# Performance work log

Hardware: AMD Instinct MI355X
Metric: run time of the kernel (lower is better)

The kernel has to match this reference:

```python
import jax, jax.numpy as jnp
import numpy as np

DIM = 64; Hh = 128; Ww = 128; Bz = 4
N = 8      # d_state
R = 4      # dt_rank = ceil(dim/16)
K = 4      # depthwise conv kernel
NB = 4     # number of CrossMambaBlocks (spa, spe, spa_cross, spe_cross)


def setup_inputs() -> dict:
    key = jax.random.key(0)
    ks = jax.random.split(key, 16)
    f32 = jnp.float32
    D = DIM
    rn = lambda k, shp, s: jax.random.normal(k, shp, f32) * s
    inp = {
        "img1": rn(ks[0], (Bz, D, Hh, Ww), 1.0),
        "img2": rn(ks[1], (Bz, D, Hh, Ww), 1.0),
        "img1_sum": rn(ks[2], (Bz, D, Hh, Ww), 1.0),
        "img2_sum": rn(ks[3], (Bz, D, Hh, Ww), 1.0),
        # LayerNorm params for norm0/norm1 of each block
        "ln_g0": jnp.ones((NB, D), f32), "ln_b0": jnp.zeros((NB, D), f32),
        "ln_g1": jnp.ones((NB, D), f32), "ln_b1": jnp.zeros((NB, D), f32),
        # Mamba projections (in_proj -> x,z from input0; in_proj_e -> extra embedding path)
        "W_in": rn(ks[4], (NB, D, 2 * D), D ** -0.5),
        "W_ine": rn(ks[5], (NB, D, D), D ** -0.5),
        # per-direction depthwise causal conv
        "convW": rn(ks[6], (NB, 2, D, K), K ** -0.5),
        "convB": jnp.zeros((NB, 2, D), f32),
        # x_proj (dt, B, C) computed from the cross-modal embedding (v7 cross variant)
        "W_x": rn(ks[7], (NB, 2, D, R + 2 * N), D ** -0.5),
        "W_dt": rn(ks[8], (NB, 2, R, D), R ** -0.5),
        "b_dt": jnp.full((NB, 2, D), -4.6, f32),  # softplus ~ 0.01
        "A_log": jnp.log(jnp.broadcast_to(jnp.arange(1, N + 1, dtype=f32), (NB, 2, D, N))),
        "Dp": jnp.ones((NB, 2, D), f32),
        "W_out": rn(ks[9], (NB, D, D), D ** -0.5),
        "b_out": jnp.zeros((NB, D), f32),
        # FusionMamba.out_proj
        "W_fo": rn(ks[10], (D, D), D ** -0.5),
        "b_fo": jnp.zeros((D,), f32),
    }
    return inp


def _ln(x, g, b):
    m = x.mean(-1, keepdims=True)
    v = ((x - m) ** 2).mean(-1, keepdims=True)
    return (x - m) * jax.lax.rsqrt(v + 1e-5) * g + b


def _causal_conv(x, w, b):
    # x: [B, L, D], w: [D, K] depthwise causal conv
    xt = x.transpose(0, 2, 1)  # [B, D, L]
    out = jax.lax.conv_general_dilated(xt, w[:, None, :], (1,), [(K - 1, 0)],
                                       feature_group_count=w.shape[0])
    return out.transpose(0, 2, 1) + b


def _selective_scan(x, dt, Bm, Cm, A):
    # x, dt: [B, L, D]; Bm, Cm: [B, L, N]; A: [D, N]
    def step(h, t):
        x_t, dt_t, B_t, C_t = t  # [B,D],[B,D],[B,N],[B,N]
        dA = jnp.exp(dt_t[:, :, None] * A)                       # [B,D,N]
        h = h * dA + (dt_t * x_t)[:, :, None] * B_t[:, None, :]  # [B,D,N]
        y = jnp.einsum('bdn,bn->bd', h, C_t)
        return h, y
    h0 = jnp.zeros((x.shape[0], x.shape[2], A.shape[1]), x.dtype)
    xs = (x.transpose(1, 0, 2), dt.transpose(1, 0, 2),
          Bm.transpose(1, 0, 2), Cm.transpose(1, 0, 2))
    _, ys = jax.lax.scan(step, h0, xs)
    return ys.transpose(1, 0, 2)  # [B, L, D]


def _cross_mamba_block(x0, x1, i, p):
    # x0, x1: [B, L, D]; bidirectional cross Mamba (bimamba v7, sum of directions)
    skip = x0
    a = _ln(x0, p['ln_g0'][i], p['ln_b0'][i])
    e = _ln(x1, p['ln_g1'][i], p['ln_b1'][i])
    xz = a @ p['W_in'][i]
    x, z = jnp.split(xz, 2, axis=-1)
    ee = e @ p['W_ine'][i]  # cross-modal embedding drives dt/B/C
    y = 0.0
    for d in range(2):
        xd = x if d == 0 else x[:, ::-1]
        ed = ee if d == 0 else ee[:, ::-1]
        zd = z if d == 0 else z[:, ::-1]
        xc = jax.nn.silu(_causal_conv(xd, p['convW'][i, d], p['convB'][i, d]))
        dbl = ed @ p['W_x'][i, d]
        dtr, Bm, Cm = dbl[..., :R], dbl[..., R:R + N], dbl[..., R + N:]
        dt = jax.nn.softplus(dtr @ p['W_dt'][i, d] + p['b_dt'][i, d])
        A = -jnp.exp(p['A_log'][i, d])
        yd = _selective_scan(xc, dt, Bm, Cm, A) + xc * p['Dp'][i, d]
        yd = yd * jax.nn.silu(zd)
        if d == 1:
            yd = yd[:, ::-1]
        y = y + yd
    return y @ p['W_out'][i] + p['b_out'][i] + skip


def reference(img1, img2, img1_sum, img2_sum, ln_g0, ln_b0, ln_g1, ln_b1,
              W_in, W_ine, convW, convB, W_x, W_dt, b_dt, A_log, Dp,
              W_out, b_out, W_fo, b_fo):
    p = dict(ln_g0=ln_g0, ln_b0=ln_b0, ln_g1=ln_g1, ln_b1=ln_b1, W_in=W_in,
             W_ine=W_ine, convW=convW, convB=convB, W_x=W_x, W_dt=W_dt,
             b_dt=b_dt, A_log=A_log, Dp=Dp, W_out=W_out, b_out=b_out)
    b, c, h, w = img1.shape
    flat = lambda t: t.reshape(b, c, h * w).transpose(0, 2, 1)   # b c h w -> b (hw) c
    unflat = lambda t: t.transpose(0, 2, 1).reshape(b, c, h, w)
    x1, x2, s1, s2 = flat(img1), flat(img2), flat(img1_sum), flat(img2_sum)
    x1 = _cross_mamba_block(x1, s1, 0, p)  # spa layer
    x2 = _cross_mamba_block(x2, s2, 1, p)  # spe layer
    spa = _cross_mamba_block(x1, x2, 2, p)
    spe = _cross_mamba_block(x2, x1, 3, p)
    fusion = (spa + spe) @ W_fo + b_fo
    out = unflat(fusion)
    return (unflat(x1) + out, unflat(x2) + out, img1_sum, img2_sum)
```

## Files before the change

### kernel.cpp

```cpp
#include <hip/hip_runtime.h>
#include <hip/hip_bf16.h>

#define BZ 4
#define DD 64
#define LL 16384
#define NN 8
#define BLD ((size_t)BZ*DD*LL)
#define BML ((size_t)BZ*20*LL)

__device__ __forceinline__ float silu_(float x){ return __fdividef(x, 1.f + __expf(-x)); }
__device__ __forceinline__ float softplus_(float x){ return (x > 20.f) ? x : __logf(1.f + __expf(x)); }


__global__ __launch_bounds__(256)
void k_tr(const float* __restrict__ t0, const float* __restrict__ t1,
          const float* __restrict__ t2, const float* __restrict__ t3,
          float* __restrict__ d0, float* __restrict__ d1,
          float* __restrict__ d2, float* __restrict__ d3)
{
  __shared__ float tile[64][65];
  const int tid = blockIdx.x;
  const int tsr = tid >> 10;
  const int rem = tid & 1023;
  const int b  = rem >> 8;
  const int l0 = (rem & 255) << 6;
  const float* s = (tsr==0)?t0:(tsr==1)?t1:(tsr==2)?t2:t3;
  float*       d = (tsr==0)?d0:(tsr==1)?d1:(tsr==2)?d2:d3;
  const int w = threadIdx.x >> 6, lane = threadIdx.x & 63;
  #pragma unroll
  for (int i=0;i<16;++i){
    const int ch = w*16+i;
    tile[ch][lane] = s[((size_t)(b*DD+ch))*LL + l0 + lane];
  }
  __syncthreads();
  #pragma unroll
  for (int i=0;i<16;++i){
    const int lw = w*16+i;
    d[((size_t)b*LL + l0+lw)*DD + lane] = tile[lane][lw];
  }
}

__global__ __launch_bounds__(256)
void k_in2(const float* __restrict__ s0a, const float* __restrict__ s1a,
           const float* __restrict__ s0b, const float* __restrict__ s1b,
           const float* __restrict__ lng0, const float* __restrict__ lnb0,
           const float* __restrict__ lng1, const float* __restrict__ lnb1,
           const float* __restrict__ W_in, const float* __restrict__ W_ine,
           const float* __restrict__ W_x, int i0,
           float* __restrict__ XBa, float* __restrict__ ZBa,
           float* __restrict__ XBb, float* __restrict__ ZBb,
           float* __restrict__ M00, float* __restrict__ M01,
           float* __restrict__ M10, float* __restrict__ M11)
{
  const int sel  = blockIdx.x >> 8;
  const int pi   = sel / 3;
  const int role = sel - 3*pi;
  const int pos = (blockIdx.x & 255)*256 + threadIdx.x;
  const int b = pos >> 14;
  const int l = pos & (LL-1);
  const int i = i0 + pi;
  const size_t row = ((size_t)b*LL + l)*DD;

  if (role < 2){
    const float* src0 = pi ? s0b : s0a;
    float a[DD];
    {
      const float4* s4 = (const float4*)(src0 + row);
      #pragma unroll
      for (int q=0;q<16;++q){ float4 v=s4[q]; a[4*q]=v.x; a[4*q+1]=v.y; a[4*q+2]=v.z; a[4*q+3]=v.w; }
    }
    float m=0.f;
    #pragma unroll
    for (int k=0;k<DD;++k) m += a[k];
    m *= (1.f/DD);
    float v=0.f;
    #pragma unroll
    for (int k=0;k<DD;++k){ float d=a[k]-m; v += d*d; }
    v *= (1.f/DD);
    const float rs = rsqrtf(v + 1e-5f);
    #pragma unroll
    for (int k=0;k<DD;++k) a[k] = (a[k]-m)*rs*lng0[i*DD+k] + lnb0[i*DD+k];

    const float* Wi = W_in + (size_t)i*DD*2*DD;
    float* drow = ((role==0) ? (pi ? XBb : XBa) : (pi ? ZBb : ZBa)) + row;
    const int gbase = role*4;
    for (int g=0; g<4; ++g){
      float acc[16];
      #pragma unroll
      for (int j=0;j<16;++j) acc[j]=0.f;
      #pragma unroll
      for (int k=0;k<DD;++k){
        const float av = a[k];
        const float* wr = Wi + k*128 + (gbase+g)*16;
        #pragma unroll
        for (int j=0;j<16;++j) acc[j] = fmaf(av, wr[j], acc[j]);
      }
      #pragma unroll
      for (int q=0;q<4;++q)
        ((float4*)(drow + g*16))[q] = make_float4(acc[4*q],acc[4*q+1],acc[4*q+2],acc[4*q+3]);
    }
  } else {
    const float* src1 = pi ? s1b : s1a;
    float e[DD];
    {
      const float4* s4 = (const float4*)(src1 + row);
      #pragma unroll
      for (int q=0;q<16;++q){ float4 v=s4[q]; e[4*q]=v.x; e[4*q+1]=v.y; e[4*q+2]=v.z; e[4*q+3]=v.w; }
    }
    float m=0.f;
    #pragma unroll
    for (int k=0;k<DD;++k) m += e[k];
    m *= (1.f/DD);
    float v=0.f;
    #pragma unroll
    for (int k=0;k<DD;++k){ float d=e[k]-m; v += d*d; }
    v *= (1.f/DD);
    const float rs = rsqrtf(v + 1e-5f);
    #pragma unroll
    for (int k=0;k<DD;++k) e[k] = (e[k]-m)*rs*lng1[i*DD+k] + lnb1[i*DD+k];

    const float* We  = W_ine + (size_t)i*DD*DD;
    const float* Wx0 = W_x + ((size_t)(i*2+0)*DD)*20;
    const float* Wx1 = W_x + ((size_t)(i*2+1)*DD)*20;
    float acc0[20], acc1[20];
    #pragma unroll
    for (int j=0;j<20;++j){ acc0[j]=0.f; acc1[j]=0.f; }
    for (int gg=0; gg<4; ++gg){
      float eeg[16];
      #pragma unroll
      for (int j=0;j<16;++j) eeg[j]=0.f;
      #pragma unroll
      for (int k=0;k<DD;++k){
        const float ev = e[k];
        const float* wr = We + k*DD + gg*16;
        #pragma unroll
        for (int j=0;j<16;++j) eeg[j] = fmaf(ev, wr[j], eeg[j]);
      }
      const float* w0 = Wx0 + (size_t)(gg*16)*20;
      const float* w1 = Wx1 + (size_t)(gg*16)*20;
      #pragma unroll
      for (int jj=0;jj<16;++jj){
        const float s = eeg[jj];
        #pragma unroll
        for (int j=0;j<20;++j){
          acc0[j] = fmaf(s, w0[jj*20+j], acc0[j]);
          acc1[j] = fmaf(s, w1[jj*20+j], acc1[j]);
        }
      }
    }
    float* mrow0 = (pi ? M10 : M00) + ((size_t)b*LL + l)*20;
    float* mrow1 = (pi ? M11 : M01) + ((size_t)b*LL + l)*20;
    #pragma unroll
    for (int q=0;q<5;++q){
      ((float4*)mrow0)[q] = make_float4(acc0[4*q],acc0[4*q+1],acc0[4*q+2],acc0[4*q+3]);
      ((float4*)mrow1)[q] = make_float4(acc1[4*q],acc1[4*q+1],acc1[4*q+2],acc1[4*q+3]);
    }
  }
}

template<int NC2, bool PASSC>
__global__ __launch_bounds__(64)
void k_scan4(const float* __restrict__ XBa, const float* __restrict__ XBb,
             const float* __restrict__ ZBa, const float* __restrict__ ZBb,
             float* __restrict__ Y0, float* __restrict__ Y1,
             float* __restrict__ Y2, float* __restrict__ Y3,
             const float* __restrict__ M00, const float* __restrict__ M01,
             const float* __restrict__ M10, const float* __restrict__ M11,
             const float* __restrict__ convW, const float* __restrict__ convB,
             const float* __restrict__ Wdt, const float* __restrict__ bdt,
             const float* __restrict__ Alog, const float* __restrict__ Dpw, int i0,
             float* __restrict__ PP, float* __restrict__ FF,
             const float* __restrict__ HH)
{
  const int TC2 = LL / NC2;
  const size_t SC2 = (size_t)BZ*NC2*DD*NN;
  const int inst = blockIdx.x / (BZ*NC2);
  const int rb = blockIdx.x - inst*(BZ*NC2);
  const int c = rb & (NC2-1);
  const int b = rb / NC2;
  const int ch = threadIdx.x;
  const int pi = inst >> 1, d = inst & 1;
  const int id = (i0+pi)*2 + d;

  const float* xb = pi ? XBb : XBa;
  const float* zb = pi ? ZBb : ZBa;
  const float* meta = (inst==0)?M00:(inst==1)?M01:(inst==2)?M10:M11;
  float* yb = (inst==0)?Y0:(inst==1)?Y1:(inst==2)?Y2:Y3;

  float cw[4];
  #pragma unroll
  for (int k=0;k<4;++k) cw[k] = convW[((size_t)id*DD+ch)*4 + k];
  const float cb = convB[id*DD + ch];
  float wd[4];
  #pragma unroll
  for (int r=0;r<4;++r) wd[r] = Wdt[((size_t)id*4 + r)*DD + ch];
  const float bd = bdt[id*DD + ch];
  float An[NN];
  #pragma unroll
  for (int n=0;n<NN;++n) An[n] = -__expf(Alog[((size_t)id*DD+ch)*NN + n]);
  const float dp = PASSC ? Dpw[id*DD + ch] : 0.f;

  bool fastA = true;
  #pragma unroll
  for (int n=0;n<NN;++n) fastA = fastA && (fabsf(An[n] + (float)(n+1)) < 1e-3f);

  const size_t sbase = (size_t)inst*SC2 + ((size_t)(b*NC2+c)*DD + ch)*NN;
  float h[NN], P[NN];
  float Sdt = 0.f;
  if (PASSC){
    #pragma unroll
    for (int n=0;n<NN;++n) h[n] = HH[sbase+n];
  } else {
    #pragma unroll
    for (int n=0;n<NN;++n){ h[n]=0.f; P[n]=1.f; }
  }

  const int stp = d ? -1 : 1;
  const int t0  = d ? (LL-1 - c*TC2) : (c*TC2);

  float p1=0.f, p2=0.f, p3=0.f;
  {
    int tp = t0 - stp;
    if ((unsigned)tp < LL) p1 = xb[((size_t)b*LL+tp)*DD+ch];
    tp -= stp;
    if ((unsigned)tp < LL) p2 = xb[((size_t)b*LL+tp)*DD+ch];
    tp -= stp;
    if ((unsigned)tp < LL) p3 = xb[((size_t)b*LL+tp)*DD+ch];
  }

  int t = t0;
  for (int s=0; s<TC2; ++s, t+=stp){
    const size_t row = (size_t)b*LL + t;
    const float xv = xb[row*DD+ch];
    const float xc = silu_(cb + cw[0]*p3 + cw[1]*p2 + cw[2]*p1 + cw[3]*xv);
    p3=p2; p2=p1; p1=xv;

    const float* mt = meta + row*20;
    const float dpre = bd + mt[0]*wd[0] + mt[1]*wd[1] + mt[2]*wd[2] + mt[3]*wd[3];
    const float dt = softplus_(dpre);
    const float u = dt*xc;

    float dA[NN];
    if (fastA){
      const float E = __expf(-dt);
      const float E2 = E*E, E4 = E2*E2;
      dA[0]=E;    dA[1]=E2;    dA[2]=E2*E;  dA[3]=E4;
      dA[4]=E4*E; dA[5]=E4*E2; dA[6]=E4*E2*E; dA[7]=E4*E4;
      Sdt += dt;
    } else {
      #pragma unroll
      for (int n=0;n<NN;++n) dA[n] = __expf(dt*An[n]);
    }

    if (!PASSC){
      #pragma unroll
      for (int n=0;n<NN;++n) h[n] = fmaf(h[n], dA[n], u*mt[4+n]);
      if (!fastA){
        #pragma unroll
        for (int n=0;n<NN;++n) P[n] *= dA[n];
      }
    } else {
      float y = 0.f;
      #pragma unroll
      for (int n=0;n<NN;++n){
        h[n] = fmaf(h[n], dA[n], u*mt[4+n]);
        y = fmaf(h[n], mt[12+n], y);
      }
      const float zv = zb[row*DD+ch];
      yb[row*DD + ch] = (y + xc*dp)*silu_(zv);
    }
  }

  if (!PASSC){
    if (fastA){
      const float E = __expf(-Sdt);
      const float E2 = E*E, E4 = E2*E2;
      P[0]=E;    P[1]=E2;    P[2]=E2*E;  P[3]=E4;
      P[4]=E4*E; P[5]=E4*E2; P[6]=E4*E2*E; P[7]=E4*E4;
    }
    #pragma unroll
    for (int n=0;n<NN;++n){ PP[sbase+n] = P[n]; FF[sbase+n] = h[n]; }
  }
}

template<int NC2>
__global__ __launch_bounds__(256)
void k_mid4(const float* __restrict__ PP, const float* __restrict__ FF,
            float* __restrict__ HH)
{
  const size_t SC2 = (size_t)BZ*NC2*DD*NN;
  const int inst = blockIdx.x >> 3;
  const int idx = (blockIdx.x & 7)*256 + threadIdx.x;
  const int b  = idx >> 9;
  const int cn = idx & 511;
  const size_t base = (size_t)inst*SC2;
  float h = 0.f;
  #pragma unroll 4
  for (int c=0; c<NC2; ++c){
    const size_t a2 = base + (((size_t)(b*NC2+c))<<9) + cn;
    HH[a2] = h;
    h = h*PP[a2] + FF[a2];
  }
}

__global__ __launch_bounds__(256)
void k_out2(const float* __restrict__ Y0, const float* __restrict__ Y1,
            const float* __restrict__ Y2, const float* __restrict__ Y3,
            const float* __restrict__ skipA, const float* __restrict__ skipB,
            const float* __restrict__ Wout, const float* __restrict__ bout,
            float* __restrict__ dstA, float* __restrict__ dstB)
{
  const int sel = blockIdx.x >> 8;
  const int pi = sel >> 2;
  const int g  = sel & 3;
  const int pos = (blockIdx.x & 255)*256 + threadIdx.x;
  const int b = pos >> 14;
  const int l = pos & (LL-1);
  const size_t row = ((size_t)b*LL + l)*DD;

  const float* Ya = pi ? Y2 : Y0;
  const float* Yb = pi ? Y3 : Y1;
  const float* skip = pi ? skipB : skipA;
  float* dst = pi ? dstB : dstA;
  const float* Wo = Wout + (size_t)pi*DD*DD;
  const float* bo = bout + pi*DD;

  float y[DD];
  {
    const float4* pa = (const float4*)(Ya + row);
    const float4* pb = (const float4*)(Yb + row);
    #pragma unroll
    for (int q=0;q<16;++q){
      float4 v0=pa[q], v1=pb[q];
      y[4*q]=v0.x+v1.x; y[4*q+1]=v0.y+v1.y; y[4*q+2]=v0.z+v1.z; y[4*q+3]=v0.w+v1.w;
    }
  }
  float acc[16];
  #pragma unroll
  for (int j=0;j<16;++j) acc[j]=0.f;
  #pragma unroll
  for (int k=0;k<DD;++k){
    const float av = y[k];
    const float* wr = Wo + k*DD + g*16;
    #pragma unroll
    for (int j=0;j<16;++j) acc[j] = fmaf(av, wr[j], acc[j]);
  }
  const float4* sk4 = (const float4*)(skip + row + g*16);
  float4* d4 = (float4*)(dst + row + g*16);
  #pragma unroll
  for (int q=0;q<4;++q){
    float4 sv = sk4[q];
    float4 v;
    v.x = acc[4*q+0] + bo[g*16+4*q+0] + sv.x;
    v.y = acc[4*q+1] + bo[g*16+4*q+1] + sv.y;
    v.z = acc[4*q+2] + bo[g*16+4*q+2] + sv.z;
    v.w = acc[4*q+3] + bo[g*16+4*q+3] + sv.w;
    d4[q] = v;
  }
}

__global__ __launch_bounds__(256)
void k_o34(const float* __restrict__ Y0, const float* __restrict__ Y1,
           const float* __restrict__ Y2, const float* __restrict__ Y3,
           const float* __restrict__ X1, const float* __restrict__ X2,
           const float* __restrict__ Wout, const float* __restrict__ bout,
           float* __restrict__ FSa, float* __restrict__ FSb)
{
  const int sel = blockIdx.x >> 8;
  const int wh = sel >> 2;
  const int g  = sel & 3;
  const int pos = (blockIdx.x & 255)*256 + threadIdx.x;
  const int b = pos >> 14;
  const int l = pos & (LL-1);
  const size_t row = ((size_t)b*LL + l)*DD;

  const float* Ya = wh ? Y2 : Y0;
  const float* Yb = wh ? Y3 : Y1;
  const float* skip = wh ? X2 : X1;
  float* FS = wh ? FSb : FSa;
  const float* Wo = Wout + (size_t)(2+wh)*DD*DD;
  const float* bo = bout + (2+wh)*DD;

  float y[DD];
  {
    const float4* pa = (const float4*)(Ya + row);
    const float4* pb = (const float4*)(Yb + row);
    #pragma unroll
    for (int q=0;q<16;++q){
      float4 v0=pa[q], v1=pb[q];
      y[4*q]=v0.x+v1.x; y[4*q+1]=v0.y+v1.y; y[4*q+2]=v0.z+v1.z; y[4*q+3]=v0.w+v1.w;
    }
  }
  float acc[16];
  #pragma unroll
  for (int j=0;j<16;++j) acc[j]=0.f;
  #pragma unroll
  for (int k=0;k<DD;++k){
    const float av = y[k];
    const float* wr = Wo + k*DD + g*16;
    #pragma unroll
    for (int j=0;j<16;++j) acc[j] = fmaf(av, wr[j], acc[j]);
  }
  const float4* sk4 = (const float4*)(skip + row + g*16);
  float4* f4 = (float4*)(FS + row + g*16);
  #pragma unroll
  for (int q=0;q<4;++q){
    float4 sv = sk4[q];
    float4 v;
    v.x = acc[4*q+0] + bo[g*16+4*q+0] + sv.x;
    v.y = acc[4*q+1] + bo[g*16+4*q+1] + sv.y;
    v.z = acc[4*q+2] + bo[g*16+4*q+2] + sv.z;
    v.w = acc[4*q+3] + bo[g*16+4*q+3] + sv.w;
    f4[q] = v;
  }
}

__global__ __launch_bounds__(256)
void k_fuse2(const float* __restrict__ FSa, const float* __restrict__ FSb,
             const float* __restrict__ X1, const float* __restrict__ X2,
             const float* __restrict__ Wfo, const float* __restrict__ bfo,
             float* __restrict__ ob)
{
  const int g = blockIdx.x >> 8;
  const int pos = (blockIdx.x & 255)*256 + threadIdx.x;
  const int b = pos >> 14;
  const int l = pos & (LL-1);
  const size_t row = ((size_t)b*LL + l)*DD;

  float fs[DD];
  {
    const float4* pa = (const float4*)(FSa + row);
    const float4* pb = (const float4*)(FSb + row);
    #pragma unroll
    for (int q=0;q<16;++q){
      float4 v0=pa[q], v1=pb[q];
      fs[4*q]=v0.x+v1.x; fs[4*q+1]=v0.y+v1.y; fs[4*q+2]=v0.z+v1.z; fs[4*q+3]=v0.w+v1.w;
    }
  }
  float acc[16];
  #pragma unroll
  for (int j=0;j<16;++j) acc[j]=0.f;
  #pragma unroll
  for (int k=0;k<DD;++k){
    const float av = fs[k];
    const float* wr = Wfo + k*DD + g*16;
    #pragma unroll
    for (int j=0;j<16;++j) acc[j] = fmaf(av, wr[j], acc[j]);
  }
  float x1v[16], x2v[16];
  {
    const float4* p1 = (const float4*)(X1 + row + g*16);
    const float4* p2 = (const float4*)(X2 + row + g*16);
    #pragma unroll
    for (int q=0;q<4;++q){
      float4 v1=p1[q], v2=p2[q];
      x1v[4*q]=v1.x; x1v[4*q+1]=v1.y; x1v[4*q+2]=v1.z; x1v[4*q+3]=v1.w;
      x2v[4*q]=v2.x; x2v[4*q+1]=v2.y; x2v[4*q+2]=v2.z; x2v[4*q+3]=v2.w;
    }
  }
  #pragma unroll
  for (int j=0;j<16;++j){
    const int col = g*16 + j;
    const size_t o = ((size_t)(b*DD+col))*LL + l;
    const float fu = acc[j] + bfo[col];
    ob[o]       = x1v[j] + fu;
    ob[BLD + o] = x2v[j] + fu;
  }
}

__global__ __launch_bounds__(256)
void k_copyboth(const float* __restrict__ s1, const float* __restrict__ s2,
                float* __restrict__ o)
{
  const size_t gid = (size_t)blockIdx.x*256 + threadIdx.x;
  const size_t half = BLD/4;
  if (gid < half) ((float4*)(o        ))[gid]        = ((const float4*)s1)[gid];
  else            ((float4*)(o + BLD ))[gid - half]  = ((const float4*)s2)[gid - half];
}

__global__ __launch_bounds__(256)
void k_copy4(const float* __restrict__ s, float* __restrict__ o)
{
  const size_t i = (size_t)blockIdx.x*256 + threadIdx.x;
  ((float4*)o)[i] = ((const float4*)s)[i];
}

__global__ __launch_bounds__(256)
void f_in(const float* __restrict__ src0, const float* __restrict__ src1,
          const float* __restrict__ lng0, const float* __restrict__ lnb0,
          const float* __restrict__ lng1, const float* __restrict__ lnb1,
          const float* __restrict__ W_in, const float* __restrict__ W_ine,
          const float* __restrict__ W_x, int i,
          float* __restrict__ XB, float* __restrict__ ZB,
          float* __restrict__ M0, float* __restrict__ M1)
{
  const int gid = blockIdx.x*256 + threadIdx.x;
  const int b = gid >> 14;
  const int l = gid & (LL-1);

  float a[DD];
  for (int ch=0; ch<DD; ++ch) a[ch] = src0[((size_t)(b*DD+ch))*LL + l];
  {
    float m=0.f; for (int k=0;k<DD;++k) m += a[k];  m *= (1.f/DD);
    float v=0.f; for (int k=0;k<DD;++k){ float d=a[k]-m; v += d*d; }  v *= (1.f/DD);
    float rs = rsqrtf(v + 1e-5f);
    for (int k=0;k<DD;++k) a[k] = (a[k]-m)*rs*lng0[i*DD+k] + lnb0[i*DD+k];
  }
  const float* Wi = W_in + (size_t)i*DD*2*DD;
  float* xrow = XB + ((size_t)b*LL + l)*DD;
  float* zrow = ZB + ((size_t)b*LL + l)*DD;
  for (int g=0; g<8; ++g){
    float acc[16];
    #pragma unroll
    for (int j=0;j<16;++j) acc[j]=0.f;
    for (int k=0;k<DD;++k){
      const float av = a[k];
      const float* wr = Wi + k*128 + g*16;
      #pragma unroll
      for (int j=0;j<16;++j) acc[j] = fmaf(av, wr[j], acc[j]);
    }
    float* drow = (g<4) ? (xrow + g*16) : (zrow + (g-4)*16);
    #pragma unroll
    for (int q=0;q<4;++q)
      ((float4*)drow)[q] = make_float4(acc[4*q],acc[4*q+1],acc[4*q+2],acc[4*q+3]);
  }
  float e[DD], ee[DD];
  for (int ch=0; ch<DD; ++ch) e[ch] = src1[((size_t)(b*DD+ch))*LL + l];
  {
    float m=0.f; for (int k=0;k<DD;++k) m += e[k];  m *= (1.f/DD);
    float v=0.f; for (int k=0;k<DD;++k){ float d=e[k]-m; v += d*d; }  v *= (1.f/DD);
    float rs = rsqrtf(v + 1e-5f);
    for (int k=0;k<DD;++k) e[k] = (e[k]-m)*rs*lng1[i*DD+k] + lnb1[i*DD+k];
  }
  const float* We = W_ine + (size_t)i*DD*DD;
  for (int m2=0; m2<DD; ++m2){
    float s = 0.f;
    for (int k=0;k<DD;++k) s = fmaf(e[k], We[k*DD + m2], s);
    ee[m2] = s;
  }
  for (int d=0; d<2; ++d){
    float acc[20];
    #pragma unroll
    for (int j=0;j<20;++j) acc[j]=0.f;
    for (int m2=0; m2<DD; ++m2){
      const float ev = ee[m2];
      const float* wr = W_x + ((size_t)(i*2+d)*DD + m2)*20;
      #pragma unroll
      for (int j=0;j<20;++j) acc[j] = fmaf(ev, wr[j], acc[j]);
    }
    float* mrow = (d ? M1 : M0) + ((size_t)b*LL + l)*20;
    #pragma unroll
    for (int q=0;q<5;++q)
      ((float4*)mrow)[q] = make_float4(acc[4*q],acc[4*q+1],acc[4*q+2],acc[4*q+3]);
  }
}

template<int DIR, bool PASSC>
__global__ __launch_bounds__(64)
void f_scan(const float* __restrict__ xb, const float* __restrict__ zb,
            float* __restrict__ yb, const float* __restrict__ meta,
            const float* __restrict__ convW, const float* __restrict__ convB,
            const float* __restrict__ Wdt, const float* __restrict__ bdt,
            const float* __restrict__ Alog, const float* __restrict__ Dpw, int id,
            float* __restrict__ Pb, float* __restrict__ Fb,
            const float* __restrict__ Hin)
{
  const int ch = threadIdx.x;
  const int c  = blockIdx.x & 255;
  const int b  = blockIdx.x >> 8;

  float cw[4];
  for (int k=0;k<4;++k) cw[k] = convW[((size_t)id*DD+ch)*4 + k];
  const float cb = convB[id*DD + ch];
  float wd[4]; for (int r=0;r<4;++r) wd[r] = Wdt[((size_t)id*4 + r)*DD + ch];
  const float bd = bdt[id*DD + ch];
  float An[NN]; for (int n=0;n<NN;++n) An[n] = -__expf(Alog[((size_t)id*DD+ch)*NN + n]);
  const float dp = PASSC ? Dpw[id*DD + ch] : 0.f;

  const size_t sbase = ((size_t)(b*256+c)*DD + ch)*NN;
  float h[NN], P[NN];
  if (PASSC){
    #pragma unroll
    for (int n=0;n<NN;++n) h[n] = Hin[sbase+n];
  } else {
    #pragma unroll
    for (int n=0;n<NN;++n){ h[n]=0.f; P[n]=1.f; }
  }

  int t0, stp;
  if (DIR==0){ t0 = c*64;        stp =  1; }
  else       { t0 = LL-1 - c*64; stp = -1; }

  float p1=0.f, p2=0.f, p3=0.f;
  {
    int tp = t0 - stp;
    if ((unsigned)tp < LL) p1 = xb[((size_t)b*LL+tp)*DD+ch];
    tp -= stp;
    if ((unsigned)tp < LL) p2 = xb[((size_t)b*LL+tp)*DD+ch];
    tp -= stp;
    if ((unsigned)tp < LL) p3 = xb[((size_t)b*LL+tp)*DD+ch];
  }

  int t = t0;
  for (int s=0; s<64; ++s, t+=stp){
    const size_t row = (size_t)b*LL + t;
    const float xv = xb[row*DD+ch];
    const float xc = silu_(cb + cw[0]*p3 + cw[1]*p2 + cw[2]*p1 + cw[3]*xv);
    p3=p2; p2=p1; p1=xv;

    const float* mt = meta + row*20;
    const float dpre = bd + mt[0]*wd[0] + mt[1]*wd[1] + mt[2]*wd[2] + mt[3]*wd[3];
    const float dt = softplus_(dpre);
    const float u = dt*xc;

    if (!PASSC){
      #pragma unroll
      for (int n=0;n<NN;++n){
        const float dA = __expf(dt*An[n]);
        h[n] = h[n]*dA + u*mt[4+n];
        P[n] *= dA;
      }
    } else {
      float y = 0.f;
      #pragma unroll
      for (int n=0;n<NN;++n){
        const float dA = __expf(dt*An[n]);
        h[n] = h[n]*dA + u*mt[4+n];
        y = fmaf(h[n], mt[12+n], y);
      }
      const float zv = zb[row*DD+ch];
      const float o = (y + xc*dp)*silu_(zv);
      float* yp = yb + row*DD + ch;
      if (DIR==0) *yp = o; else *yp += o;
    }
  }

  if (!PASSC){
    #pragma unroll
    for (int n=0;n<NN;++n){ Pb[sbase+n] = P[n]; Fb[sbase+n] = h[n]; }
  }
}

__global__ __launch_bounds__(256)
void f_mid(const float* __restrict__ Pb, const float* __restrict__ Fb,
           float* __restrict__ Hin)
{
  const int idx = blockIdx.x*256 + threadIdx.x;
  const int b  = idx >> 9;
  const int cn = idx & 511;
  float h = 0.f;
  #pragma unroll 4
  for (int c=0; c<256; ++c){
    const size_t a2 = (((size_t)(b*256+c))<<9) + cn;
    Hin[a2] = h;
    h = h*Pb[a2] + Fb[a2];
  }
}

template<int MODE>
__global__ __launch_bounds__(256)
void f_out(const float* __restrict__ YB, const float* __restrict__ skip,
           const float* __restrict__ Wo, const float* __restrict__ bo,
           float* __restrict__ dst)
{
  const int gid = blockIdx.x*256 + threadIdx.x;
  const int b = gid >> 14;
  const int l = gid & (LL-1);
  float y[DD];
  {
    const float4* s4 = (const float4*)(YB + ((size_t)b*LL + l)*DD);
    #pragma unroll
    for (int q=0;q<16;++q){ float4 v=s4[q]; y[4*q]=v.x; y[4*q+1]=v.y; y[4*q+2]=v.z; y[4*q+3]=v.w; }
  }
  for (int g=0; g<4; ++g){
    float acc[16];
    #pragma unroll
    for (int j=0;j<16;++j) acc[j]=0.f;
    for (int k=0;k<DD;++k){
      const float av = y[k];
      const float* wr = Wo + k*DD + g*16;
      #pragma unroll
      for (int j=0;j<16;++j) acc[j] = fmaf(av, wr[j], acc[j]);
    }
    #pragma unroll
    for (int j=0;j<16;++j){
      const int col = g*16 + j;
      const size_t o = ((size_t)(b*DD+col))*LL + l;
      float s = acc[j] + bo[col] + skip[o];
      if (MODE==1) s += dst[o];
      dst[o] = s;
    }
  }
}

__global__ __launch_bounds__(256)
void f_fuse(const float* __restrict__ FS, const float* __restrict__ X1,
            const float* __restrict__ X2, const float* __restrict__ Wfo,
            const float* __restrict__ bfo, float* __restrict__ ob)
{
  const int gid = blockIdx.x*256 + threadIdx.x;
  const int b = gid >> 14;
  const int l = gid & (LL-1);
  float fs[DD];
  for (int ch=0; ch<DD; ++ch) fs[ch] = FS[((size_t)(b*DD+ch))*LL + l];
  for (int g=0; g<4; ++g){
    float acc[16];
    #pragma unroll
    for (int j=0;j<16;++j) acc[j]=0.f;
    for (int k=0;k<DD;++k){
      const float av = fs[k];
      const float* wr = Wfo + k*DD + g*16;
      #pragma unroll
      for (int j=0;j<16;++j) acc[j] = fmaf(av, wr[j], acc[j]);
    }
    #pragma unroll
    for (int j=0;j<16;++j){
      const int col = g*16 + j;
      const size_t o = ((size_t)(b*DD+col))*LL + l;
      const float fu = acc[j] + bfo[col];
      ob[o]       = X1[o] + fu;
      ob[BLD + o] = X2[o] + fu;
    }
  }
}

extern "C" void kernel_launch(void* const* d_in, const int* in_sizes, int n_in,
                              void* d_out, int out_size, void* d_ws, size_t ws_size,
                              hipStream_t stream)
{
  static const int dictsz[21]  = {4194304,4194304,4194304,4194304,256,256,256,256,
                                  32768,16384,2048,512,10240,2048,512,4096,512,
                                  16384,256,4096,64};
  int map[21];
  bool okd = (n_in >= 21);
  if (okd) for (int i=0;i<21;++i) if (in_sizes[i] != dictsz[i]) { okd = false; break; }
  if (okd){
    for (int i=0;i<21;++i) map[i] = i;
  } else {
    bool used[64];
    for (int j=0;j<64;++j) used[j]=false;
    for (int i=0;i<21;++i){
      map[i] = -1;
      for (int j=0;j<n_in && j<64;++j)
        if (!used[j] && in_sizes[j]==dictsz[i]){ map[i]=j; used[j]=true; break; }
      if (map[i] < 0) map[i] = (i < n_in ? i : 0);
    }
  }

  const float* img1 = (const float*)d_in[map[0]];
  const float* img2 = (const float*)d_in[map[1]];
  const float* s1   = (const float*)d_in[map[2]];
  const float* s2   = (const float*)d_in[map[3]];
  const float* lng0 = (const float*)d_in[map[4]];
  const float* lnb0 = (const float*)d_in[map[5]];
  const float* lng1 = (const float*)d_in[map[6]];
  const float* lnb1 = (const float*)d_in[map[7]];
  const float* Win  = (const float*)d_in[map[8]];
  const float* Wine = (const float*)d_in[map[9]];
  const float* convW= (const float*)d_in[map[10]];
  const float* convB= (const float*)d_in[map[11]];
  const float* Wx   = (const float*)d_in[map[12]];
  const float* Wdt  = (const float*)d_in[map[13]];
  const float* bdt  = (const float*)d_in[map[14]];
  const float* Alog = (const float*)d_in[map[15]];
  const float* Dp   = (const float*)d_in[map[16]];
  const float* Wout = (const float*)d_in[map[17]];
  const float* bout = (const float*)d_in[map[18]];
  const float* Wfo  = (const float*)d_in[map[19]];
  const float* bfo  = (const float*)d_in[map[20]];

  float* ob = (float*)d_out;
  float* ws = (float*)d_ws;

  const size_t SCN512 = (size_t)BZ*512*DD*NN;
  const size_t SCN256 = (size_t)BZ*256*DD*NN;
  const size_t need512 = (10*BLD + 4*BML + 12*SCN512 + 64)*sizeof(float);
  const size_t need256 = (10*BLD + 4*BML + 12*SCN256 + 64)*sizeof(float);

  if (ws_size >= need256){
    k_copyboth<<<8192,256,0,stream>>>(s1, s2, ob + 2*BLD);

    const bool big = (ws_size >= need512);
    const size_t SC = big ? SCN512 : SCN256;
    float* X1  = ws;
    float* X2  = ws + 1*BLD;
    float* XBa = ws + 2*BLD;
    float* ZBa = ws + 3*BLD;
    float* XBb = ws + 4*BLD;
    float* ZBb = ws + 5*BLD;
    float* Y0  = ws + 6*BLD;
    float* Y1  = ws + 7*BLD;
    float* Y2  = ws + 8*BLD;
    float* Y3  = ws + 9*BLD;
    float* M00 = ws + 10*BLD;
    float* M01 = M00 + BML;
    float* M10 = M01 + BML;
    float* M11 = M10 + BML;
    float* PP  = M11 + BML;
    float* FF  = PP + 4*SC;
    float* HH  = FF + 4*SC;

    k_tr<<<4096,256,0,stream>>>(img1, img2, s1, s2, X1, X2, Y0, Y1);

    for (int pr=0; pr<2; ++pr){
      const int i0 = pr*2;
      if (pr==0)
        k_in2<<<1536,256,0,stream>>>(X1, Y0, X2, Y1, lng0,lnb0,lng1,lnb1,
                                     Win, Wine, Wx, 0, XBa,ZBa,XBb,ZBb, M00,M01,M10,M11);
      else
        k_in2<<<1536,256,0,stream>>>(X1, X2, X2, X1, lng0,lnb0,lng1,lnb1,
                                     Win, Wine, Wx, 2, XBa,ZBa,XBb,ZBb, M00,M01,M10,M11);
      if (big){
        k_scan4<512,false><<<4*BZ*512,64,0,stream>>>(XBa,XBb,ZBa,ZBb, Y0,Y1,Y2,Y3,
                                                     M00,M01,M10,M11, convW,convB,Wdt,bdt,Alog,Dp,
                                                     i0, PP,FF,HH);
        k_mid4<512><<<32,256,0,stream>>>(PP,FF,HH);
        k_scan4<512,true ><<<4*BZ*512,64,0,stream>>>(XBa,XBb,ZBa,ZBb, Y0,Y1,Y2,Y3,
                                                     M00,M01,M10,M11, convW,convB,Wdt,bdt,Alog,Dp,
                                                     i0, PP,FF,HH);
      } else {
        k_scan4<256,false><<<4*BZ*256,64,0,stream>>>(XBa,XBb,ZBa,ZBb, Y0,Y1,Y2,Y3,
                                                     M00,M01,M10,M11, convW,convB,Wdt,bdt,Alog,Dp,
                                                     i0, PP,FF,HH);
        k_mid4<256><<<32,256,0,stream>>>(PP,FF,HH);
        k_scan4<256,true ><<<4*BZ*256,64,0,stream>>>(XBa,XBb,ZBa,ZBb, Y0,Y1,Y2,Y3,
                                                     M00,M01,M10,M11, convW,convB,Wdt,bdt,Alog,Dp,
                                                     i0, PP,FF,HH);
      }
      if (pr==0){
        k_out2<<<2048,256,0,stream>>>(Y0,Y1,Y2,Y3, X1,X2, Wout,bout, X1,X2);
      } else {
        k_o34<<<2048,256,0,stream>>>(Y0,Y1,Y2,Y3, X1,X2, Wout,bout, XBa, ZBa);
        k_fuse2<<<1024,256,0,stream>>>(XBa, ZBa, X1, X2, Wfo, bfo, ob);
      }
    }
    return;
  }

  k_copy4<<<4096,256,0,stream>>>(s1, ob + 2*BLD);
  k_copy4<<<4096,256,0,stream>>>(s2, ob + 3*BLD);

  float* X1 = ws;
  float* X2 = ws + 1*BLD;
  float* FS = ws + 2*BLD;
  float* XB = ws + 3*BLD;
  float* ZB = ws + 4*BLD;
  float* YB = ws + 5*BLD;
  float* M0 = ws + 6*BLD;
  float* M1 = M0 + BML;
  float* PP = M1 + BML;
  float* FF = PP + SCN256;
  float* HH = FF + SCN256;

  const size_t need = (6*BLD + 2*BML + 3*SCN256 + 64)*sizeof(float);
  if (ws_size < need) return;

  const float* bx0[4] = {img1, img2, X1, X2};
  const float* bx1[4] = {s1,   s2,   X2, X1};

  for (int i=0; i<4; ++i){
    f_in<<<256,256,0,stream>>>(bx0[i], bx1[i], lng0, lnb0, lng1, lnb1,
                               Win, Wine, Wx, i, XB, ZB, M0, M1);
    for (int d=0; d<2; ++d){
      const int id = i*2+d;
      const float* Md = d ? M1 : M0;
      if (d==0){
        f_scan<0,false><<<BZ*256,64,0,stream>>>(XB,nullptr,nullptr,Md,convW,convB,Wdt,bdt,Alog,nullptr,id,PP,FF,nullptr);
        f_mid<<<8,256,0,stream>>>(PP,FF,HH);
        f_scan<0,true ><<<BZ*256,64,0,stream>>>(XB,ZB,YB,Md,convW,convB,Wdt,bdt,Alog,Dp,id,nullptr,nullptr,HH);
      } else {
        f_scan<1,false><<<BZ*256,64,0,stream>>>(XB,nullptr,nullptr,Md,convW,convB,Wdt,bdt,Alog,nullptr,id,PP,FF,nullptr);
        f_mid<<<8,256,0,stream>>>(PP,FF,HH);
        f_scan<1,true ><<<BZ*256,64,0,stream>>>(XB,ZB,YB,Md,convW,convB,Wdt,bdt,Alog,Dp,id,nullptr,nullptr,HH);
      }
    }
    const float* Wop = Wout + (size_t)i*DD*DD;
    const float* bop = bout + (size_t)i*DD;
    if      (i==0) f_out<0><<<256,256,0,stream>>>(YB, img1, Wop, bop, X1);
    else if (i==1) f_out<0><<<256,256,0,stream>>>(YB, img2, Wop, bop, X2);
    else if (i==2) f_out<0><<<256,256,0,stream>>>(YB, X1,   Wop, bop, FS);
    else           f_out<1><<<256,256,0,stream>>>(YB, X2,   Wop, bop, FS);
  }
  f_fuse<<<256,256,0,stream>>>(FS, X1, X2, Wfo, bfo, ob);
}
```

Before: 857.3 us.

## Fuse sum-image transpose into input projection and tile it through shared memory

The transpose of the two sum images is folded into the input-projection kernel, which now reads them in channel-major layout through a shared-memory tile. That removes one full write and read of two BLD tensors. The projection kernel is rebuilt so each 256-thread block handles 64 positions, with 4 threads per position splitting the output columns. The outputs are staged in shared memory for coalesced stores, where each thread used to compute a whole row alone from 64 registers. The extra-embedding path also splits the x_proj work across threads, which reduces the redundant per-thread compute and register pressure. The cost is more block-wide syncs and more shared-memory traffic per block.

```diff
diff --git a/kernel.cpp b/kernel.cpp
--- a/kernel.cpp
+++ b/kernel.cpp
@@ -13,10 +13,8 @@
 
 
 __global__ __launch_bounds__(256)
-void k_tr(const float* __restrict__ t0, const float* __restrict__ t1,
-          const float* __restrict__ t2, const float* __restrict__ t3,
-          float* __restrict__ d0, float* __restrict__ d1,
-          float* __restrict__ d2, float* __restrict__ d3)
+void k_tr2(const float* __restrict__ t0, const float* __restrict__ t1,
+           float* __restrict__ d0, float* __restrict__ d1)
 {
   __shared__ float tile[64][65];
   const int tid = blockIdx.x;
@@ -24,8 +22,8 @@
   const int rem = tid & 1023;
   const int b  = rem >> 8;
   const int l0 = (rem & 255) << 6;
-  const float* s = (tsr==0)?t0:(tsr==1)?t1:(tsr==2)?t2:t3;
-  float*       d = (tsr==0)?d0:(tsr==1)?d1:(tsr==2)?d2:d3;
+  const float* s = tsr ? t1 : t0;
+  float*       d = tsr ? d1 : d0;
   const int w = threadIdx.x >> 6, lane = threadIdx.x & 63;
   #pragma unroll
   for (int i=0;i<16;++i){
@@ -41,8 +39,9 @@
 }
 
 __global__ __launch_bounds__(256)
-void k_in2(const float* __restrict__ s0a, const float* __restrict__ s1a,
-           const float* __restrict__ s0b, const float* __restrict__ s1b,
+void k_in3(const float* __restrict__ A0, const float* __restrict__ A1,
+           const float* __restrict__ E0, const float* __restrict__ E1,
+           int etin,
            const float* __restrict__ lng0, const float* __restrict__ lnb0,
            const float* __restrict__ lng1, const float* __restrict__ lnb1,
            const float* __restrict__ W_in, const float* __restrict__ W_ine,
@@ -52,109 +51,103 @@
            float* __restrict__ M00, float* __restrict__ M01,
            float* __restrict__ M10, float* __restrict__ M11)
 {
-  const int sel  = blockIdx.x >> 8;
-  const int pi   = sel / 3;
-  const int role = sel - 3*pi;
-  const int pos = (blockIdx.x & 255)*256 + threadIdx.x;
-  const int b = pos >> 14;
-  const int l = pos & (LL-1);
+  __shared__ float tin[64][65];
+  __shared__ float tou[64][65];
+  const int fam = blockIdx.x >> 10;
+  const int blk = blockIdx.x & 1023;
+  const int pi = fam >> 1, path = fam & 1;
+  const int b  = blk >> 8;
+  const int l0 = (blk & 255) << 6;
   const int i = i0 + pi;
-  const size_t row = ((size_t)b*LL + l)*DD;
-
-  if (role < 2){
-    const float* src0 = pi ? s0b : s0a;
-    float a[DD];
-    {
-      const float4* s4 = (const float4*)(src0 + row);
-      #pragma unroll
-      for (int q=0;q<16;++q){ float4 v=s4[q]; a[4*q]=v.x; a[4*q+1]=v.y; a[4*q+2]=v.z; a[4*q+3]=v.w; }
-    }
-    float m=0.f;
-    #pragma unroll
-    for (int k=0;k<DD;++k) m += a[k];
-    m *= (1.f/DD);
-    float v=0.f;
-    #pragma unroll
-    for (int k=0;k<DD;++k){ float d=a[k]-m; v += d*d; }
-    v *= (1.f/DD);
-    const float rs = rsqrtf(v + 1e-5f);
-    #pragma unroll
-    for (int k=0;k<DD;++k) a[k] = (a[k]-m)*rs*lng0[i*DD+k] + lnb0[i*DD+k];
-
+  const int tid = threadIdx.x;
+  const int p = tid >> 2, sub = tid & 3;
+
+  const float* src = (path==0) ? (pi?A1:A0) : (pi?E1:E0);
+  if (path==1 && etin){
+    const int lane = tid & 63, chb = tid >> 6;
+    #pragma unroll
+    for (int it=0; it<16; ++it){
+      const int ch = chb*16 + it;
+      tin[ch][lane] = src[((size_t)(b*DD+ch))*LL + l0 + lane];
+    }
+  } else {
+    #pragma unroll
+    for (int it=0; it<16; ++it){
+      const int f = it*256 + tid;
+      const int row = f >> 6, col = f & 63;
+      tin[col][row] = src[((size_t)b*LL + l0 + row)*DD + col];
+    }
+  }
+  __syncthreads();
+
+  float m=0.f;
+  #pragma unroll
+  for (int k=0;k<DD;++k) m += tin[k][p];
+  m *= (1.f/DD);
+  float v=0.f;
+  #pragma unroll
+  for (int k=0;k<DD;++k){ float d=tin[k][p]-m; v += d*d; }
+  v *= (1.f/DD);
+  const float rs = rsqrtf(v + 1e-5f);
+  const float* gw = (path==0)? (lng0 + i*DD) : (lng1 + i*DD);
+  const float* bw = (path==0)? (lnb0 + i*DD) : (lnb1 + i*DD);
+
+  if (path==0){
     const float* Wi = W_in + (size_t)i*DD*2*DD;
-    float* drow = ((role==0) ? (pi ? XBb : XBa) : (pi ? ZBb : ZBa)) + row;
-    const int gbase = role*4;
-    for (int g=0; g<4; ++g){
+    for (int h=0; h<2; ++h){
       float acc[16];
       #pragma unroll
       for (int j=0;j<16;++j) acc[j]=0.f;
       #pragma unroll
       for (int k=0;k<DD;++k){
-        const float av = a[k];
-        const float* wr = Wi + k*128 + (gbase+g)*16;
+        const float a = fmaf((tin[k][p]-m)*rs, gw[k], bw[k]);
+        const float* wr = Wi + k*128 + h*64 + sub*16;
         #pragma unroll
-        for (int j=0;j<16;++j) acc[j] = fmaf(av, wr[j], acc[j]);
+        for (int j=0;j<16;++j) acc[j] = fmaf(a, wr[j], acc[j]);
       }
       #pragma unroll
-      for (int q=0;q<4;++q)
-        ((float4*)(drow + g*16))[q] = make_float4(acc[4*q],acc[4*q+1],acc[4*q+2],acc[4*q+3]);
+      for (int j=0;j<16;++j) tou[p][sub*16+j] = acc[j];
+      __syncthreads();
+      float* D = h ? (pi?ZBb:ZBa) : (pi?XBb:XBa);
+      #pragma unroll
+      for (int it=0; it<16; ++it){
+        const int f = it*256 + tid;
+        const int row = f>>6, col = f&63;
+        D[((size_t)b*LL + l0 + row)*DD + col] = tou[row][col];
+      }
+      __syncthreads();
     }
   } else {
-    const float* src1 = pi ? s1b : s1a;
-    float e[DD];
-    {
-      const float4* s4 = (const float4*)(src1 + row);
-      #pragma unroll
-      for (int q=0;q<16;++q){ float4 v=s4[q]; e[4*q]=v.x; e[4*q+1]=v.y; e[4*q+2]=v.z; e[4*q+3]=v.w; }
-    }
-    float m=0.f;
-    #pragma unroll
-    for (int k=0;k<DD;++k) m += e[k];
-    m *= (1.f/DD);
-    float v=0.f;
-    #pragma unroll
-    for (int k=0;k<DD;++k){ float d=e[k]-m; v += d*d; }
-    v *= (1.f/DD);
-    const float rs = rsqrtf(v + 1e-5f);
-    #pragma unroll
-    for (int k=0;k<DD;++k) e[k] = (e[k]-m)*rs*lng1[i*DD+k] + lnb1[i*DD+k];
-
-    const float* We  = W_ine + (size_t)i*DD*DD;
-    const float* Wx0 = W_x + ((size_t)(i*2+0)*DD)*20;
-    const float* Wx1 = W_x + ((size_t)(i*2+1)*DD)*20;
-    float acc0[20], acc1[20];
-    #pragma unroll
-    for (int j=0;j<20;++j){ acc0[j]=0.f; acc1[j]=0.f; }
-    for (int gg=0; gg<4; ++gg){
-      float eeg[16];
-      #pragma unroll
-      for (int j=0;j<16;++j) eeg[j]=0.f;
-      #pragma unroll
-      for (int k=0;k<DD;++k){
-        const float ev = e[k];
-        const float* wr = We + k*DD + gg*16;
-        #pragma unroll
-        for (int j=0;j<16;++j) eeg[j] = fmaf(ev, wr[j], eeg[j]);
-      }
-      const float* w0 = Wx0 + (size_t)(gg*16)*20;
-      const float* w1 = Wx1 + (size_t)(gg*16)*20;
-      #pragma unroll
-      for (int jj=0;jj<16;++jj){
-        const float s = eeg[jj];
-        #pragma unroll
-        for (int j=0;j<20;++j){
-          acc0[j] = fmaf(s, w0[jj*20+j], acc0[j]);
-          acc1[j] = fmaf(s, w1[jj*20+j], acc1[j]);
-        }
-      }
-    }
-    float* mrow0 = (pi ? M10 : M00) + ((size_t)b*LL + l)*20;
-    float* mrow1 = (pi ? M11 : M01) + ((size_t)b*LL + l)*20;
-    #pragma unroll
-    for (int q=0;q<5;++q){
-      ((float4*)mrow0)[q] = make_float4(acc0[4*q],acc0[4*q+1],acc0[4*q+2],acc0[4*q+3]);
-      ((float4*)mrow1)[q] = make_float4(acc1[4*q],acc1[4*q+1],acc1[4*q+2],acc1[4*q+3]);
-    }
+    const float* We = W_ine + (size_t)i*DD*DD;
+    float acc[16];
+    #pragma unroll
+    for (int j=0;j<16;++j) acc[j]=0.f;
+    #pragma unroll
+    for (int k=0;k<DD;++k){
+      const float e = fmaf((tin[k][p]-m)*rs, gw[k], bw[k]);
+      const float* wr = We + k*DD + sub*16;
+      #pragma unroll
+      for (int j=0;j<16;++j) acc[j] = fmaf(e, wr[j], acc[j]);
+    }
+    #pragma unroll
+    for (int j=0;j<16;++j) tou[p][sub*16+j] = acc[j];
+    __syncthreads();
+    const int d = sub>>1, cbase = (sub&1)*10;
+    const float* Wx = W_x + ((size_t)(i*2+d)*DD)*20;
+    float mac[10];
+    #pragma unroll
+    for (int j=0;j<10;++j) mac[j]=0.f;
+    #pragma unroll
+    for (int k=0;k<DD;++k){
+      const float ee = tou[p][k];
+      const float* wr = Wx + k*20 + cbase;
+      #pragma unroll
+      for (int j=0;j<10;++j) mac[j] = fmaf(ee, wr[j], mac[j]);
+    }
+    float* M = pi? (d?M11:M10) : (d?M01:M00);
+    float* mrow = M + ((size_t)b*LL + l0 + p)*20 + cbase;
+    #pragma unroll
+    for (int j=0;j<10;++j) mrow[j] = mac[j];
   }
 }
 
@@ -800,15 +793,15 @@
     float* FF  = PP + 4*SC;
     float* HH  = FF + 4*SC;
 
-    k_tr<<<4096,256,0,stream>>>(img1, img2, s1, s2, X1, X2, Y0, Y1);
+    k_tr2<<<2048,256,0,stream>>>(img1, img2, X1, X2);
 
     for (int pr=0; pr<2; ++pr){
       const int i0 = pr*2;
       if (pr==0)
-        k_in2<<<1536,256,0,stream>>>(X1, Y0, X2, Y1, lng0,lnb0,lng1,lnb1,
+        k_in3<<<4096,256,0,stream>>>(X1, X2, s1, s2, 1, lng0,lnb0,lng1,lnb1,
                                      Win, Wine, Wx, 0, XBa,ZBa,XBb,ZBb, M00,M01,M10,M11);
       else
-        k_in2<<<1536,256,0,stream>>>(X1, X2, X2, X1, lng0,lnb0,lng1,lnb1,
+        k_in3<<<4096,256,0,stream>>>(X1, X2, X2, X1, 0, lng0,lnb0,lng1,lnb1,
                                      Win, Wine, Wx, 2, XBa,ZBa,XBb,ZBb, M00,M01,M10,M11);
       if (big){
         k_scan4<512,false><<<4*BZ*512,64,0,stream>>>(XBa,XBb,ZBa,ZBb, Y0,Y1,Y2,Y3,
```

After: 1.566 ms. +82.6%, slower.
